# Performance work log

Measured on AMD Instinct MI355X. Metric: run time of the kernel, lower is better.

Reference implementation:

```python
import jax, jax.numpy as jnp
import numpy as np

EMBED = 1024
FF = 4096
LN_EPS = 1e-5

def _layernorm(x, gamma, beta):
    mu = jnp.mean(x, axis=-1, keepdims=True)
    var = jnp.var(x, axis=-1, keepdims=True)
    return (x - mu) * jax.lax.rsqrt(var + LN_EPS) * gamma + beta

def setup_inputs() -> dict:
    key = jax.random.key(0)
    ks = jax.random.split(key, 16)
    s = 1.0 / np.sqrt(EMBED)
    s2 = 1.0 / np.sqrt(FF)
    return {
        "x": jax.random.normal(ks[0], (8, 2048, EMBED), dtype=jnp.float32),
        "Wq": jax.random.uniform(ks[1], (EMBED, EMBED), jnp.float32, -s, s),
        "bq": jnp.zeros((EMBED,), jnp.float32),
        "Wk": jax.random.uniform(ks[2], (EMBED, EMBED), jnp.float32, -s, s),
        "bk": jnp.zeros((EMBED,), jnp.float32),
        "Wv": jax.random.uniform(ks[3], (EMBED, EMBED), jnp.float32, -s, s),
        "bv": jnp.zeros((EMBED,), jnp.float32),
        "Wo": jax.random.uniform(ks[4], (EMBED, EMBED), jnp.float32, -s, s),
        "bo": jnp.zeros((EMBED,), jnp.float32),
        "g1": jnp.ones((EMBED,), jnp.float32),
        "b1": jnp.zeros((EMBED,), jnp.float32),
        "g2": jnp.ones((EMBED,), jnp.float32),
        "b2": jnp.zeros((EMBED,), jnp.float32),
        "W1": jax.random.uniform(ks[5], (EMBED, FF), jnp.float32, -s, s),
        "bf1": jnp.zeros((FF,), jnp.float32),
        "W2": jax.random.uniform(ks[6], (FF, EMBED), jnp.float32, -s2, s2),
        "bf2": jnp.zeros((EMBED,), jnp.float32),
    }

def reference(x, Wq, bq, Wk, bk, Wv, bv, Wo, bo, g1, b1, g2, b2, W1, bf1, W2, bf2):
    # Single-head attention (heads arg unused in original forward)
    Q = jnp.einsum('bse,ef->bsf', x, Wq) + bq
    K = jnp.einsum('bse,ef->bsf', x, Wk) + bk
    V = jnp.einsum('bse,ef->bsf', x, Wv) + bv
    scale = 1.0 / jnp.sqrt(jnp.float32(EMBED))
    scores = jnp.einsum('bqe,bke->bqk', Q, K) * scale  # [B,S,S]
    attn = jax.nn.softmax(scores, axis=-1)
    attn_out = jnp.einsum('bqk,bke->bqe', attn, V)
    attn_out = jnp.einsum('bse,ef->bsf', attn_out, Wo) + bo
    # dropout is identity in eval mode
    h = _layernorm(x + attn_out, g1, b1)
    ffn = jnp.einsum('bsf,fh->bsh', jax.nn.relu(jnp.einsum('bse,eh->bsh', h, W1) + bf1), W2) + bf2
    return _layernorm(h + ffn, g2, b2)
```

## Files before the change

kernel.cpp:

```cpp
#include <hip/hip_runtime.h>


typedef __attribute__((ext_vector_type(4))) float  f32x4;
typedef __attribute__((ext_vector_type(8))) short  s16x8;
typedef __attribute__((ext_vector_type(4))) short  s16x4;
typedef unsigned short u16;
typedef unsigned int   u32;

__device__ __forceinline__ float bf2f(short s) {
  u32 u = ((u32)(u16)s) << 16;
  float f; __builtin_memcpy(&f, &u, 4); return f;
}
__device__ __forceinline__ short f2bf(float f) {
  u32 u; __builtin_memcpy(&u, &f, 4);
  u32 r = (u + 0x7fffu + ((u >> 16) & 1u)) >> 16;
  return (short)(u16)r;
}

__device__ __forceinline__ void gload16(const void* g, void* l) {
  __builtin_amdgcn_global_load_lds(
      (const __attribute__((address_space(1))) u32*)g,
      (__attribute__((address_space(3))) u32*)l, 16, 0, 0);
}

__device__ __forceinline__ void stage_half(const char* gop, long long ldb,
                                           long long rowbase, int tt, int h,
                                           u16* ldsop, int tid) {
#pragma unroll
  for (int l = 0; l < 2; ++l) {
    const int o   = (l * 512 + tid) * 16;
    const int rih = o >> 7;
    const int scb = (o & 127) ^ ((rih & 7) << 4);
    gload16(gop + (rowbase + h * 128 + rih) * ldb + (long long)tt * 128 + scb,
            (char*)ldsop + h * 16384 + o);
  }
}

#define SABUF(c) (SMEM + (c) * 16384)
#define SBBUF(c) (SMEM + 32768 + (c) * 16384)

#define RD_A(MH) do { _Pragma("unroll") for (int mi = 0; mi < 4; ++mi) { \
    const int row_ = wm * 64 + (MH) * 128 + mi * 16 + lr; \
    const int sw_ = (row_ & 7) << 4; const int rb_ = row_ << 7; \
    _Pragma("unroll") for (int kk = 0; kk < 2; ++kk) \
      af[mi][kk] = *(const s16x8*)(pa + rb_ + (((kk << 6) | (kg << 4)) ^ sw_)); } } while (0)

#define RD_B(NH) do { _Pragma("unroll") for (int nj = 0; nj < 2; ++nj) { \
    const int row_ = wn * 32 + (NH) * 128 + nj * 16 + lr; \
    const int sw_ = (row_ & 7) << 4; const int rb_ = row_ << 7; \
    _Pragma("unroll") for (int kk = 0; kk < 2; ++kk) \
      bf[NH][nj][kk] = *(const s16x8*)(pb + rb_ + (((kk << 6) | (kg << 4)) ^ sw_)); } } while (0)

#define MM(MH, NH) do { _Pragma("unroll") for (int kk = 0; kk < 2; ++kk) \
    _Pragma("unroll") for (int mi = 0; mi < 4; ++mi) \
    _Pragma("unroll") for (int nj = 0; nj < 2; ++nj) \
      acc[(MH) * 4 + mi][(NH) * 2 + nj] = __builtin_amdgcn_mfma_f32_16x16x32_bf16( \
        af[mi][kk], bf[NH][nj][kk], acc[(MH) * 4 + mi][(NH) * 2 + nj], 0, 0, 0); } while (0)

#define PH_SYNC do { __builtin_amdgcn_s_barrier(); \
    asm volatile("s_waitcnt lgkmcnt(0)"); \
    __builtin_amdgcn_sched_barrier(0); } while (0)

template<int MODE>
__global__ __launch_bounds__(512, 2)
void gemm256(const u16* __restrict__ A, const u16* __restrict__ BT,
             u16* __restrict__ C,
             const float* __restrict__ bias0, const float* __restrict__ bias1,
             const float* __restrict__ bias2, float* __restrict__ lsum,
             int M, int N, int K, float scale,
             long long sA, long long sB, long long sC) {
  __shared__ u16 SMEM[65536];

  const int gx = gridDim.x, gy = gridDim.y;
  const int nwg = gx * gy * gridDim.z;
  const int orig = (blockIdx.z * gy + blockIdx.y) * gx + blockIdx.x;
  const int q = nwg >> 3, r8 = nwg & 7;
  const int xcd = orig & 7, pos = orig >> 3;
  const int wg = (xcd < r8 ? xcd * (q + 1) : r8 * (q + 1) + (xcd - r8) * q) + pos;
  const int bz = wg / (gx * gy);
  const int rem = wg % (gx * gy);
  const long long bm = (long long)(rem / gx) * 256;
  const long long bn = (long long)(rem % gx) * 256;

  const char* Ag = (const char*)(A + (long long)bz * sA);
  const char* Bg = (const char*)(BT + (long long)bz * sB);
  u16* Cb = C + (long long)bz * sC;
  const long long ldb = (long long)K * 2;

  const int tid = threadIdx.x;
  const int lane = tid & 63, wid = tid >> 6;
  const int lr = lane & 15, kg = lane >> 4;
  const int wm = wid >> 2, wn = wid & 3;
  const int NT = K >> 6;

  f32x4 acc[8][4] = {};
  s16x8 af[4][2];
  s16x8 bf[2][2][2];

  stage_half(Ag, ldb, bm, 0, 0, SABUF(0), tid);
  stage_half(Bg, ldb, bn, 0, 0, SBBUF(0), tid);
  stage_half(Ag, ldb, bm, 0, 1, SABUF(0), tid);
  stage_half(Bg, ldb, bn, 0, 1, SBBUF(0), tid);
  stage_half(Ag, ldb, bm, 1, 0, SABUF(1), tid);
  stage_half(Bg, ldb, bn, 1, 0, SBBUF(1), tid);
  asm volatile("s_waitcnt vmcnt(4)");
  __builtin_amdgcn_s_barrier();

  for (int T = 0; T < NT; ++T) {
    const int c = T & 1, cn = c ^ 1;
    const char* pa = (const char*)SABUF(c);
    const char* pb = (const char*)SBBUF(c);

    RD_A(0); RD_B(0);
    if (T + 1 < NT) stage_half(Ag, ldb, bm, T + 1, 1, SABUF(cn), tid);
    PH_SYNC;
    __builtin_amdgcn_s_setprio(1); MM(0, 0); __builtin_amdgcn_s_setprio(0);
    __builtin_amdgcn_s_barrier();

    RD_B(1);
    if (T + 1 < NT) stage_half(Bg, ldb, bn, T + 1, 1, SBBUF(cn), tid);
    PH_SYNC;
    __builtin_amdgcn_s_setprio(1); MM(0, 1); __builtin_amdgcn_s_setprio(0);
    __builtin_amdgcn_s_barrier();

    RD_A(1);
    if (T + 2 < NT) stage_half(Ag, ldb, bm, T + 2, 0, SABUF(c), tid);
    PH_SYNC;
    __builtin_amdgcn_s_setprio(1); MM(1, 0); __builtin_amdgcn_s_setprio(0);
    __builtin_amdgcn_s_barrier();

    if (T + 2 < NT) stage_half(Bg, ldb, bn, T + 2, 0, SBBUF(c), tid);
    PH_SYNC;
    __builtin_amdgcn_s_setprio(1); MM(1, 1); __builtin_amdgcn_s_setprio(0);
    if (T + 2 < NT)      { asm volatile("s_waitcnt vmcnt(4)"); }
    else if (T + 1 < NT) { asm volatile("s_waitcnt vmcnt(0)"); }
    __builtin_amdgcn_s_barrier();
  }

  const long long zM = (long long)bz * M;
  u16* obase; long long ldc, bnl;
  const float* bptr = bias0;
  if (MODE == 5) {
    const int sel = (int)(bn >> 10);
    obase = C + (long long)sel * 16777216;
    ldc = 1024; bnl = bn & 1023;
    bptr = (sel == 0 ? bias0 : sel == 1 ? bias1 : bias2);
  } else { obase = Cb; ldc = N; bnl = bn; }

#pragma unroll
  for (int nh = 0; nh < 2; ++nh)
#pragma unroll
    for (int nj = 0; nj < 2; ++nj) {
      const int col = wn * 32 + nh * 128 + nj * 16 + lr;
      float bv = 0.f;
      if (MODE == 1 || MODE == 2 || MODE == 5) bv = bptr[bnl + col];
#pragma unroll
      for (int mh = 0; mh < 2; ++mh)
#pragma unroll
        for (int mi = 0; mi < 4; ++mi) {
          const int row0 = wm * 64 + mh * 128 + mi * 16 + kg * 4;
#pragma unroll
          for (int r = 0; r < 4; ++r) {
            float v = acc[mh * 4 + mi][nh * 2 + nj][r];
            if (MODE == 1 || MODE == 2 || MODE == 5) v = v * scale + bv;
            if (MODE == 2) v = fmaxf(v, 0.f);
            if (MODE == 3) v = __expf(v * scale);
            if (MODE == 4) v = v / lsum[zM + bm + row0 + r];
            SMEM[(row0 + r) * 256 + (col ^ (kg << 4))] = (u16)f2bf(v);
          }
        }
    }
  __syncthreads();
#pragma unroll
  for (int i = 0; i < 16; ++i) {
    const int o   = (i * 512 + tid) * 16;
    const int row = o >> 9;
    const int wb  = o & 511;
    const int gs  = (wb >> 4) ^ (((row >> 2) & 3) << 1);
    s16x8 d = *(const s16x8*)((const char*)SMEM + row * 512 + (gs << 4));
    if (MODE == 3) {
      float s = 0.f;
#pragma unroll
      for (int j = 0; j < 8; ++j) s += bf2f(d[j]);
#pragma unroll
      for (int off = 1; off < 32; off <<= 1) s += __shfl_xor(s, off);
      if ((lane & 31) == 0) atomicAdd(&lsum[zM + bm + row], s);
    }
    *(s16x8*)((char*)obase + (((long long)bm + row) * ldc + bnl) * 2 + wb) = d;
  }
}

__global__ __launch_bounds__(256) void prep(
    const float* __restrict__ x,  u16* __restrict__ XB,
    const float* __restrict__ Wq, const float* __restrict__ Wk,
    const float* __restrict__ Wv, const float* __restrict__ Wo,
    const float* __restrict__ W1, const float* __restrict__ W2,
    u16* __restrict__ WQT, u16* __restrict__ WKT, u16* __restrict__ WVT,
    u16* __restrict__ WOT, u16* __restrict__ W1T, u16* __restrict__ W2T) {
  __shared__ float tile[32][33];
  const int bid = blockIdx.x;
  const int t = threadIdx.x;
  if (bid < 16384) {
    const long long i = (long long)bid * 256 + t;
    f32x4 v = ((const f32x4*)x)[i];
    s16x4 o;
#pragma unroll
    for (int j = 0; j < 4; j++) o[j] = f2bf(v[j]);
    ((s16x4*)XB)[i] = o;
    return;
  }
  const float* in; u16* out; int R, C, tb;
  if (bid < 20480) {
    const int w = (bid - 16384) >> 10;
    tb = (bid - 16384) & 1023;
    in  = (w == 0 ? Wq : w == 1 ? Wk : w == 2 ? Wv : Wo);
    out = (w == 0 ? WQT : w == 1 ? WKT : w == 2 ? WVT : WOT);
    R = 1024; C = 1024;
  } else if (bid < 24576) {
    tb = bid - 20480; in = W1; out = W1T; R = 1024; C = 4096;
  } else {
    tb = bid - 24576; in = W2; out = W2T; R = 4096; C = 1024;
  }
  const int tpr = C >> 5;
  const int r0 = (tb / tpr) * 32, c0 = (tb % tpr) * 32;
  const int tx = t & 31, ty = t >> 5;
#pragma unroll
  for (int i = 0; i < 32; i += 8)
    tile[ty + i][tx] = in[(long long)(r0 + ty + i) * C + (c0 + tx)];
  __syncthreads();
#pragma unroll
  for (int i = 0; i < 32; i += 8)
    out[(long long)(c0 + ty + i) * R + (r0 + tx)] = (u16)f2bf(tile[tx][ty + i]);
}

__global__ __launch_bounds__(256) void transpose_bf16_bf16(const u16* __restrict__ in,
                                                           u16* __restrict__ out,
                                                           int R, int C,
                                                           long long isb, long long osb) {
  __shared__ u16 tile[32][33];
  in  += (long long)blockIdx.z * isb;
  out += (long long)blockIdx.z * osb;
  const int tx = threadIdx.x, ty = threadIdx.y;
  const int r0 = blockIdx.y * 32, c0 = blockIdx.x * 32;
#pragma unroll
  for (int i = 0; i < 32; i += 8)
    tile[ty + i][tx] = in[(long long)(r0 + ty + i) * C + (c0 + tx)];
  __syncthreads();
#pragma unroll
  for (int i = 0; i < 32; i += 8)
    out[(long long)(c0 + ty + i) * R + (r0 + tx)] = tile[tx][ty + i];
}

template<bool OUTF32>
__global__ __launch_bounds__(256) void ln_add(const u16* __restrict__ a,
                                              const u16* __restrict__ b,
                                              const float* __restrict__ g,
                                              const float* __restrict__ be,
                                              void* __restrict__ outp) {
  const long long row = blockIdx.x;
  const int t = threadIdx.x;
  s16x4 avv = ((const s16x4*)(a + row * 1024))[t];
  s16x4 bvv = ((const s16x4*)(b + row * 1024))[t];
  float v[4]; float sum = 0.f, ss = 0.f;
#pragma unroll
  for (int j = 0; j < 4; j++) { v[j] = bf2f(avv[j]) + bf2f(bvv[j]); sum += v[j]; ss += v[j] * v[j]; }
#pragma unroll
  for (int off = 32; off > 0; off >>= 1) { sum += __shfl_xor(sum, off); ss += __shfl_xor(ss, off); }
  __shared__ float red[8];
  if ((t & 63) == 0) { red[t >> 6] = sum; red[4 + (t >> 6)] = ss; }
  __syncthreads();
  sum = (red[0] + red[1]) + (red[2] + red[3]);
  ss  = (red[4] + red[5]) + (red[6] + red[7]);
  const float mu   = sum * (1.f / 1024.f);
  const float var  = ss * (1.f / 1024.f) - mu * mu;
  const float rstd = rsqrtf(var + 1e-5f);
  if (OUTF32) {
    f32x4 o;
#pragma unroll
    for (int j = 0; j < 4; j++) {
      const int c = t * 4 + j;
      o[j] = (v[j] - mu) * rstd * g[c] + be[c];
    }
    ((f32x4*)((float*)outp + row * 1024))[t] = o;
  } else {
    s16x4 o;
#pragma unroll
    for (int j = 0; j < 4; j++) {
      const int c = t * 4 + j;
      o[j] = f2bf((v[j] - mu) * rstd * g[c] + be[c]);
    }
    *(s16x4*)&((u16*)outp)[row * 1024 + t * 4] = o;
  }
}

extern "C" void kernel_launch(void* const* d_in, const int* in_sizes, int n_in,
                              void* d_out, int out_size, void* d_ws, size_t ws_size,
                              hipStream_t stream) {
  const float* x   = (const float*)d_in[0];
  const float* Wq  = (const float*)d_in[1];
  const float* bq  = (const float*)d_in[2];
  const float* Wk  = (const float*)d_in[3];
  const float* bk  = (const float*)d_in[4];
  const float* Wv  = (const float*)d_in[5];
  const float* bv  = (const float*)d_in[6];
  const float* Wo  = (const float*)d_in[7];
  const float* bo  = (const float*)d_in[8];
  const float* g1  = (const float*)d_in[9];
  const float* b1  = (const float*)d_in[10];
  const float* g2  = (const float*)d_in[11];
  const float* b2  = (const float*)d_in[12];
  const float* W1  = (const float*)d_in[13];
  const float* bf1 = (const float*)d_in[14];
  const float* W2  = (const float*)d_in[15];
  const float* bf2 = (const float*)d_in[16];
  float* out = (float*)d_out;

  char* ws = (char*)d_ws;
  u16* wsWQT = (u16*)(ws + 0);
  u16* wsWKT = (u16*)(ws + 2097152);
  u16* wsWVT = (u16*)(ws + 4194304);
  u16* wsWOT = (u16*)(ws + 6291456);
  u16* wsW1T = (u16*)(ws + 8388608);
  u16* wsW2T = (u16*)(ws + 16777216);
  u16* wsXB  = (u16*)(ws + 25165824);
  u16* wsQ   = (u16*)(ws + 58720256);
  u16* wsK   = (u16*)(ws + 92274688);
  u16* wsV   = (u16*)(ws + 125829120);
  u16* wsVT  = (u16*)(ws + 159383552);
  u16* wsS   = (u16*)(ws + 192937984);
  u16* wsAO  = wsQ;
  u16* wsAO2 = wsS;
  u16* wsH   = (u16*)(ws + 192937984 + 33554432);
  u16* wsHID = wsXB;
  u16* wsFFN = wsS;
  float* wsLSUM = (float*)wsV;

  const dim3 tb(32, 8, 1);
  const float inv_sqrt_e = 0.03125f;
  const float* nf = nullptr;
  float* nfm = nullptr;

  prep<<<28672, 256, 0, stream>>>(x, wsXB, Wq, Wk, Wv, Wo, W1, W2,
                                  wsWQT, wsWKT, wsWVT, wsWOT, wsW1T, wsW2T);

  gemm256<5><<<dim3(12, 64, 1), 512, 0, stream>>>(wsXB, wsWQT, wsQ, bq, bk, bv, nfm,
                                                  16384, 3072, 1024, 1.f, 0, 0, 0);

  transpose_bf16_bf16<<<dim3(32, 64, 8), tb, 0, stream>>>(wsV, wsVT, 2048, 1024, 2048LL * 1024, 1024LL * 2048);
  hipMemsetAsync(wsLSUM, 0, 16384 * sizeof(float), stream);

  gemm256<3><<<dim3(8, 8, 8), 512, 0, stream>>>(wsQ, wsK, wsS, nf, nf, nf, wsLSUM,
                                                2048, 2048, 1024, inv_sqrt_e,
                                                2048LL * 1024, 2048LL * 1024, 2048LL * 2048);

  gemm256<4><<<dim3(4, 8, 8), 512, 0, stream>>>(wsS, wsVT, wsAO, nf, nf, nf, wsLSUM,
                                                2048, 1024, 2048, 1.f,
                                                2048LL * 2048, 1024LL * 2048, 2048LL * 1024);
  gemm256<1><<<dim3(4, 64, 1), 512, 0, stream>>>(wsAO, wsWOT, wsAO2, bo, nf, nf, nfm,
                                                 16384, 1024, 1024, 1.f, 0, 0, 0);

  ln_add<false><<<16384, 256, 0, stream>>>(wsXB, wsAO2, g1, b1, wsH);

  gemm256<2><<<dim3(16, 64, 1), 512, 0, stream>>>(wsH, wsW1T, wsHID, bf1, nf, nf, nfm,
                                                  16384, 4096, 1024, 1.f, 0, 0, 0);

  gemm256<1><<<dim3(4, 64, 1), 512, 0, stream>>>(wsHID, wsW2T, wsFFN, bf2, nf, nf, nfm,
                                                 16384, 1024, 4096, 1.f, 0, 0, 0);

  ln_add<true><<<16384, 256, 0, stream>>>(wsH, wsFFN, g2, b2, out);

  (void)in_sizes; (void)n_in; (void)out_size; (void)ws_size;
}
```

Baseline: 614.3 us.

## Make GEMMs persistent with cross-tile prefetch and chunked epilogue

Converts the tiled GEMM into a persistent kernel launched with 256 workgroups that loop over output tiles in XCD-aware order. The next tile's first K-slices are prefetched into shared memory while the current tile finishes. The epilogue now writes 64-row chunks through the unused halves of the shared buffers, so output stores overlap with the next tile's loads. This targets per-tile prologue and epilogue bubbles and wave-quantization tails, at the cost of more barriers and register pressure.

After: 759.5 us. +23.6%, slower.

```diff
diff --git a/kernel.cpp b/kernel.cpp
--- a/kernel.cpp
+++ b/kernel.cpp
@@ -38,6 +38,8 @@
 
 #define SABUF(c) (SMEM + (c) * 16384)
 #define SBBUF(c) (SMEM + 32768 + (c) * 16384)
+#define EP0 (SMEM + 24576)
+#define EP1 (SMEM + 57344)
 
 #define RD_A(MH) do { _Pragma("unroll") for (int mi = 0; mi < 4; ++mi) { \
     const int row_ = wm * 64 + (MH) * 128 + mi * 16 + lr; \
@@ -61,132 +63,186 @@
     asm volatile("s_waitcnt lgkmcnt(0)"); \
     __builtin_amdgcn_sched_barrier(0); } while (0)
 
+__device__ __forceinline__ int perm8(int orig, int ntiles) {
+  const int q = ntiles >> 3, r8 = ntiles & 7;
+  const int xcd = orig & 7, pos = orig >> 3;
+  return (xcd < r8 ? xcd * (q + 1) : r8 * (q + 1) + (xcd - r8) * q) + pos;
+}
+
 template<int MODE>
 __global__ __launch_bounds__(512, 2)
-void gemm256(const u16* __restrict__ A, const u16* __restrict__ BT,
-             u16* __restrict__ C,
-             const float* __restrict__ bias0, const float* __restrict__ bias1,
-             const float* __restrict__ bias2, float* __restrict__ lsum,
-             int M, int N, int K, float scale,
-             long long sA, long long sB, long long sC) {
+void gemm256p(const u16* __restrict__ A, const u16* __restrict__ BT,
+              u16* __restrict__ C,
+              const float* __restrict__ bias0, const float* __restrict__ bias1,
+              const float* __restrict__ bias2, float* __restrict__ lsum,
+              int M, int N, int K, int NBZ,
+              long long sA, long long sB, long long sC, float scale) {
   __shared__ u16 SMEM[65536];
 
-  const int gx = gridDim.x, gy = gridDim.y;
-  const int nwg = gx * gy * gridDim.z;
-  const int orig = (blockIdx.z * gy + blockIdx.y) * gx + blockIdx.x;
-  const int q = nwg >> 3, r8 = nwg & 7;
-  const int xcd = orig & 7, pos = orig >> 3;
-  const int wg = (xcd < r8 ? xcd * (q + 1) : r8 * (q + 1) + (xcd - r8) * q) + pos;
-  const int bz = wg / (gx * gy);
-  const int rem = wg % (gx * gy);
-  const long long bm = (long long)(rem / gx) * 256;
-  const long long bn = (long long)(rem % gx) * 256;
-
-  const char* Ag = (const char*)(A + (long long)bz * sA);
-  const char* Bg = (const char*)(BT + (long long)bz * sB);
-  u16* Cb = C + (long long)bz * sC;
+  const int tn = N >> 8;
+  const int tilesPerZ = (M >> 8) * tn;
+  const int ntiles = NBZ * tilesPerZ;
+  const int NT = K >> 6;
   const long long ldb = (long long)K * 2;
+  const int G = gridDim.x;
 
   const int tid = threadIdx.x;
   const int lane = tid & 63, wid = tid >> 6;
   const int lr = lane & 15, kg = lane >> 4;
   const int wm = wid >> 2, wn = wid & 3;
-  const int NT = K >> 6;
+
+  const char *curA, *curB, *nxtA, *nxtB;
+  long long curBm, curBn, nxtBm, nxtBn;
+  int curZ, nxtZ;
+  auto mk = [&](int tl, const char*& ag, const char*& bg,
+                long long& bm, long long& bn, int& z) {
+    z = tl / tilesPerZ;
+    const int rm = tl - z * tilesPerZ;
+    bm = (long long)(rm / tn) << 8;
+    bn = (long long)(rm - (rm / tn) * tn) << 8;
+    ag = (const char*)(A + (long long)z * sA);
+    bg = (const char*)(BT + (long long)z * sB);
+  };
+
+  int jt = blockIdx.x;
+  mk(perm8(jt, ntiles), curA, curB, curBm, curBn, curZ);
+  bool hasNext = (jt + G) < ntiles;
+  if (hasNext) mk(perm8(jt + G, ntiles), nxtA, nxtB, nxtBm, nxtBn, nxtZ);
+  else { nxtA = curA; nxtB = curB; nxtBm = curBm; nxtBn = curBn; nxtZ = curZ; }
 
   f32x4 acc[8][4] = {};
   s16x8 af[4][2];
   s16x8 bf[2][2][2];
 
-  stage_half(Ag, ldb, bm, 0, 0, SABUF(0), tid);
-  stage_half(Bg, ldb, bn, 0, 0, SBBUF(0), tid);
-  stage_half(Ag, ldb, bm, 0, 1, SABUF(0), tid);
-  stage_half(Bg, ldb, bn, 0, 1, SBBUF(0), tid);
-  stage_half(Ag, ldb, bm, 1, 0, SABUF(1), tid);
-  stage_half(Bg, ldb, bn, 1, 0, SBBUF(1), tid);
+  stage_half(curA, ldb, curBm, 0, 0, SABUF(0), tid);
+  stage_half(curB, ldb, curBn, 0, 0, SBBUF(0), tid);
+  stage_half(curA, ldb, curBm, 0, 1, SABUF(0), tid);
+  stage_half(curB, ldb, curBn, 0, 1, SBBUF(0), tid);
+  stage_half(curA, ldb, curBm, 1, 0, SABUF(1), tid);
+  stage_half(curB, ldb, curBn, 1, 0, SBBUF(1), tid);
   asm volatile("s_waitcnt vmcnt(4)");
   __builtin_amdgcn_s_barrier();
 
-  for (int T = 0; T < NT; ++T) {
-    const int c = T & 1, cn = c ^ 1;
-    const char* pa = (const char*)SABUF(c);
-    const char* pb = (const char*)SBBUF(c);
-
-    RD_A(0); RD_B(0);
-    if (T + 1 < NT) stage_half(Ag, ldb, bm, T + 1, 1, SABUF(cn), tid);
-    PH_SYNC;
-    __builtin_amdgcn_s_setprio(1); MM(0, 0); __builtin_amdgcn_s_setprio(0);
-    __builtin_amdgcn_s_barrier();
-
-    RD_B(1);
-    if (T + 1 < NT) stage_half(Bg, ldb, bn, T + 1, 1, SBBUF(cn), tid);
-    PH_SYNC;
-    __builtin_amdgcn_s_setprio(1); MM(0, 1); __builtin_amdgcn_s_setprio(0);
-    __builtin_amdgcn_s_barrier();
-
-    RD_A(1);
-    if (T + 2 < NT) stage_half(Ag, ldb, bm, T + 2, 0, SABUF(c), tid);
-    PH_SYNC;
-    __builtin_amdgcn_s_setprio(1); MM(1, 0); __builtin_amdgcn_s_setprio(0);
-    __builtin_amdgcn_s_barrier();
-
-    if (T + 2 < NT) stage_half(Bg, ldb, bn, T + 2, 0, SBBUF(c), tid);
-    PH_SYNC;
-    __builtin_amdgcn_s_setprio(1); MM(1, 1); __builtin_amdgcn_s_setprio(0);
-    if (T + 2 < NT)      { asm volatile("s_waitcnt vmcnt(4)"); }
-    else if (T + 1 < NT) { asm volatile("s_waitcnt vmcnt(0)"); }
-    __builtin_amdgcn_s_barrier();
-  }
-
-  const long long zM = (long long)bz * M;
-  u16* obase; long long ldc, bnl;
-  const float* bptr = bias0;
-  if (MODE == 5) {
-    const int sel = (int)(bn >> 10);
-    obase = C + (long long)sel * 16777216;
-    ldc = 1024; bnl = bn & 1023;
-    bptr = (sel == 0 ? bias0 : sel == 1 ? bias1 : bias2);
-  } else { obase = Cb; ldc = N; bnl = bn; }
-
-#pragma unroll
-  for (int nh = 0; nh < 2; ++nh)
-#pragma unroll
-    for (int nj = 0; nj < 2; ++nj) {
-      const int col = wn * 32 + nh * 128 + nj * 16 + lr;
-      float bv = 0.f;
-      if (MODE == 1 || MODE == 2 || MODE == 5) bv = bptr[bnl + col];
-#pragma unroll
-      for (int mh = 0; mh < 2; ++mh)
-#pragma unroll
-        for (int mi = 0; mi < 4; ++mi) {
-          const int row0 = wm * 64 + mh * 128 + mi * 16 + kg * 4;
-#pragma unroll
-          for (int r = 0; r < 4; ++r) {
-            float v = acc[mh * 4 + mi][nh * 2 + nj][r];
-            if (MODE == 1 || MODE == 2 || MODE == 5) v = v * scale + bv;
-            if (MODE == 2) v = fmaxf(v, 0.f);
-            if (MODE == 3) v = __expf(v * scale);
-            if (MODE == 4) v = v / lsum[zM + bm + row0 + r];
-            SMEM[(row0 + r) * 256 + (col ^ (kg << 4))] = (u16)f2bf(v);
+  for (;;) {
+    for (int T = 0; T < NT; ++T) {
+      const int c = T & 1, cn = c ^ 1;
+      const char* pa = (const char*)SABUF(c);
+      const char* pb = (const char*)SBBUF(c);
+
+      const bool in1 = (T + 1 < NT), in2 = (T + 2 < NT);
+      const bool v1 = in1 || hasNext, v2 = in2 || hasNext;
+      const char* a1 = in1 ? curA : nxtA;  const char* b1 = in1 ? curB : nxtB;
+      const long long m1 = in1 ? curBm : nxtBm, n1 = in1 ? curBn : nxtBn;
+      const int tk1 = in1 ? T + 1 : 0;
+      const char* a2 = in2 ? curA : nxtA;  const char* b2 = in2 ? curB : nxtB;
+      const long long m2 = in2 ? curBm : nxtBm, n2 = in2 ? curBn : nxtBn;
+      const int tk2 = in2 ? T + 2 : T + 2 - NT;
+
+      RD_A(0); RD_B(0);
+      if (v1) stage_half(a1, ldb, m1, tk1, 1, SABUF(cn), tid);
+      PH_SYNC;
+      __builtin_amdgcn_s_setprio(1); MM(0, 0); __builtin_amdgcn_s_setprio(0);
+      __builtin_amdgcn_s_barrier();
+
+      RD_B(1);
+      if (v1) stage_half(b1, ldb, n1, tk1, 1, SBBUF(cn), tid);
+      PH_SYNC;
+      __builtin_amdgcn_s_setprio(1); MM(0, 1); __builtin_amdgcn_s_setprio(0);
+      __builtin_amdgcn_s_barrier();
+
+      RD_A(1);
+      if (v2) stage_half(a2, ldb, m2, tk2, 0, SABUF(c), tid);
+      PH_SYNC;
+      __builtin_amdgcn_s_setprio(1); MM(1, 0); __builtin_amdgcn_s_setprio(0);
+      __builtin_amdgcn_s_barrier();
+
+      if (v2) stage_half(b2, ldb, n2, tk2, 0, SBBUF(c), tid);
+      PH_SYNC;
+      __builtin_amdgcn_s_setprio(1); MM(1, 1); __builtin_amdgcn_s_setprio(0);
+      if (v2)      { asm volatile("s_waitcnt vmcnt(4)"); }
+      else if (v1) { asm volatile("s_waitcnt vmcnt(0)"); }
+      __builtin_amdgcn_s_barrier();
+    }
+
+    {
+      u16* Cb = C + (long long)curZ * sC;
+      const long long zM = (long long)curZ * M;
+      u16* obase; long long ldc, bnl;
+      const float* bptr = bias0;
+      if (MODE == 5) {
+        const int sel = (int)(curBn >> 10);
+        obase = C + (long long)sel * 16777216;
+        ldc = 1024; bnl = curBn & 1023;
+        bptr = (sel == 0 ? bias0 : sel == 1 ? bias1 : bias2);
+      } else { obase = Cb; ldc = N; bnl = curBn; }
+
+      float bvv[2][2];
+      if (MODE == 1 || MODE == 2 || MODE == 5) {
+#pragma unroll
+        for (int nh = 0; nh < 2; ++nh)
+#pragma unroll
+          for (int nj = 0; nj < 2; ++nj)
+            bvv[nh][nj] = bptr[bnl + wn * 32 + nh * 128 + nj * 16 + lr];
+      }
+
+#pragma unroll
+      for (int b = 0; b < 4; ++b) {
+        const int mh = b >> 1;
+        if (wm == (b & 1)) {
+#pragma unroll
+          for (int nh = 0; nh < 2; ++nh)
+#pragma unroll
+            for (int nj = 0; nj < 2; ++nj) {
+              const int col = wn * 32 + nh * 128 + nj * 16 + lr;
+#pragma unroll
+              for (int mi = 0; mi < 4; ++mi)
+#pragma unroll
+                for (int r = 0; r < 4; ++r) {
+                  const int lrow = mi * 16 + kg * 4 + r;
+                  float v = acc[mh * 4 + mi][nh * 2 + nj][r];
+                  if (MODE == 1 || MODE == 2 || MODE == 5) v = v * scale + bvv[nh][nj];
+                  if (MODE == 2) v = fmaxf(v, 0.f);
+                  if (MODE == 3) v = __expf(v * scale);
+                  if (MODE == 4) v = v / lsum[zM + curBm + b * 64 + lrow];
+                  u16* ep = (lrow < 32) ? EP0 : EP1;
+                  ep[(lrow & 31) * 256 + (col ^ (kg << 4))] = (u16)f2bf(v);
+                }
+            }
+        }
+        asm volatile("s_waitcnt lgkmcnt(0)" ::: "memory");
+        __builtin_amdgcn_sched_barrier(0);
+        __builtin_amdgcn_s_barrier();
+#pragma unroll
+        for (int i = 0; i < 4; ++i) {
+          const int o    = (i * 512 + tid) * 16;
+          const int lrow = o >> 9;
+          const int wb   = o & 511;
+          const int gs   = (wb >> 4) ^ (((lrow >> 2) & 3) << 1);
+          const u16* ep  = (lrow < 32) ? EP0 : EP1;
+          s16x8 d = *(const s16x8*)((const char*)ep + (lrow & 31) * 512 + (gs << 4));
+          if (MODE == 3) {
+            float s = 0.f;
+#pragma unroll
+            for (int j = 0; j < 8; ++j) s += bf2f(d[j]);
+#pragma unroll
+            for (int off = 1; off < 32; off <<= 1) s += __shfl_xor(s, off);
+            if ((lane & 31) == 0) atomicAdd(&lsum[zM + curBm + b * 64 + lrow], s);
           }
+          *(s16x8*)((char*)obase + (((long long)curBm + b * 64 + lrow) * ldc + bnl) * 2 + wb) = d;
         }
+        __builtin_amdgcn_s_barrier();
+      }
     }
-  __syncthreads();
-#pragma unroll
-  for (int i = 0; i < 16; ++i) {
-    const int o   = (i * 512 + tid) * 16;
-    const int row = o >> 9;
-    const int wb  = o & 511;
-    const int gs  = (wb >> 4) ^ (((row >> 2) & 3) << 1);
-    s16x8 d = *(const s16x8*)((const char*)SMEM + row * 512 + (gs << 4));
-    if (MODE == 3) {
-      float s = 0.f;
-#pragma unroll
-      for (int j = 0; j < 8; ++j) s += bf2f(d[j]);
-#pragma unroll
-      for (int off = 1; off < 32; off <<= 1) s += __shfl_xor(s, off);
-      if ((lane & 31) == 0) atomicAdd(&lsum[zM + bm + row], s);
-    }
-    *(s16x8*)((char*)obase + (((long long)bm + row) * ldc + bnl) * 2 + wb) = d;
+
+    jt += G;
+    if (jt >= ntiles) break;
+    curA = nxtA; curB = nxtB; curBm = nxtBm; curBn = nxtBn; curZ = nxtZ;
+    hasNext = (jt + G) < ntiles;
+    if (hasNext) mk(perm8(jt + G, ntiles), nxtA, nxtB, nxtBm, nxtBn, nxtZ);
+#pragma unroll
+    for (int i = 0; i < 8; ++i)
+#pragma unroll
+      for (int j = 0; j < 4; ++j) acc[i][j] = (f32x4){0.f, 0.f, 0.f, 0.f};
   }
 }
 
@@ -343,29 +399,30 @@
   prep<<<28672, 256, 0, stream>>>(x, wsXB, Wq, Wk, Wv, Wo, W1, W2,
                                   wsWQT, wsWKT, wsWVT, wsWOT, wsW1T, wsW2T);
 
-  gemm256<5><<<dim3(12, 64, 1), 512, 0, stream>>>(wsXB, wsWQT, wsQ, bq, bk, bv, nfm,
-                                                  16384, 3072, 1024, 1.f, 0, 0, 0);
+  gemm256p<5><<<256, 512, 0, stream>>>(wsXB, wsWQT, wsQ, bq, bk, bv, nfm,
+                                       16384, 3072, 1024, 1, 0, 0, 0, 1.f);
 
   transpose_bf16_bf16<<<dim3(32, 64, 8), tb, 0, stream>>>(wsV, wsVT, 2048, 1024, 2048LL * 1024, 1024LL * 2048);
   hipMemsetAsync(wsLSUM, 0, 16384 * sizeof(float), stream);
 
-  gemm256<3><<<dim3(8, 8, 8), 512, 0, stream>>>(wsQ, wsK, wsS, nf, nf, nf, wsLSUM,
-                                                2048, 2048, 1024, inv_sqrt_e,
-                                                2048LL * 1024, 2048LL * 1024, 2048LL * 2048);
-
-  gemm256<4><<<dim3(4, 8, 8), 512, 0, stream>>>(wsS, wsVT, wsAO, nf, nf, nf, wsLSUM,
-                                                2048, 1024, 2048, 1.f,
-                                                2048LL * 2048, 1024LL * 2048, 2048LL * 1024);
-  gemm256<1><<<dim3(4, 64, 1), 512, 0, stream>>>(wsAO, wsWOT, wsAO2, bo, nf, nf, nfm,
-                                                 16384, 1024, 1024, 1.f, 0, 0, 0);
+  gemm256p<3><<<256, 512, 0, stream>>>(wsQ, wsK, wsS, nf, nf, nf, wsLSUM,
+                                       2048, 2048, 1024, 8,
+                                       2048LL * 1024, 2048LL * 1024, 2048LL * 2048, inv_sqrt_e);
+
+  gemm256p<4><<<256, 512, 0, stream>>>(wsS, wsVT, wsAO, nf, nf, nf, wsLSUM,
+                                       2048, 1024, 2048, 8,
+                                       2048LL * 2048, 1024LL * 2048, 2048LL * 1024, 1.f);
+
+  gemm256p<1><<<256, 512, 0, stream>>>(wsAO, wsWOT, wsAO2, bo, nf, nf, nfm,
+                                       16384, 1024, 1024, 1, 0, 0, 0, 1.f);
 
   ln_add<false><<<16384, 256, 0, stream>>>(wsXB, wsAO2, g1, b1, wsH);
 
-  gemm256<2><<<dim3(16, 64, 1), 512, 0, stream>>>(wsH, wsW1T, wsHID, bf1, nf, nf, nfm,
-                                                  16384, 4096, 1024, 1.f, 0, 0, 0);
-
-  gemm256<1><<<dim3(4, 64, 1), 512, 0, stream>>>(wsHID, wsW2T, wsFFN, bf2, nf, nf, nfm,
-                                                 16384, 1024, 4096, 1.f, 0, 0, 0);
+  gemm256p<2><<<256, 512, 0, stream>>>(wsH, wsW1T, wsHID, bf1, nf, nf, nfm,
+                                       16384, 4096, 1024, 1, 0, 0, 0, 1.f);
+
+  gemm256p<1><<<256, 512, 0, stream>>>(wsHID, wsW2T, wsFFN, bf2, nf, nf, nfm,
+                                       16384, 1024, 4096, 1, 0, 0, 0, 1.f);
 
   ln_add<true><<<16384, 256, 0, stream>>>(wsH, wsFFN, g2, b2, out);
 
```

## Compute V transposed directly via swapped-operand GEMM, drop transpose kernel

Applied to the files above, without the earlier changes.

The fused QKV projection now computes only Q and K. V^T is produced directly by a new batched GEMM mode that multiplies Wv^T by the activations and adds a per-row bias. This removes the separate bf16 transpose kernel and the write and re-read of V. It relies on MODE 5's output layout placing K at the old wsK offset. It also adds a second, smaller GEMM launch with different tiling.

Result: no change. 603.8 us (-1.7%).

```diff
diff --git a/kernel.cpp b/kernel.cpp
--- a/kernel.cpp
+++ b/kernel.cpp
@@ -166,6 +166,7 @@
             if (MODE == 2) v = fmaxf(v, 0.f);
             if (MODE == 3) v = __expf(v * scale);
             if (MODE == 4) v = v / lsum[zM + bm + row0 + r];
+            if (MODE == 6) v = v * scale + bias0[bm + row0 + r];
             SMEM[(row0 + r) * 256 + (col ^ (kg << 4))] = (u16)f2bf(v);
           }
         }
@@ -231,24 +232,6 @@
 #pragma unroll
   for (int i = 0; i < 32; i += 8)
     out[(long long)(c0 + ty + i) * R + (r0 + tx)] = (u16)f2bf(tile[tx][ty + i]);
-}
-
-__global__ __launch_bounds__(256) void transpose_bf16_bf16(const u16* __restrict__ in,
-                                                           u16* __restrict__ out,
-                                                           int R, int C,
-                                                           long long isb, long long osb) {
-  __shared__ u16 tile[32][33];
-  in  += (long long)blockIdx.z * isb;
-  out += (long long)blockIdx.z * osb;
-  const int tx = threadIdx.x, ty = threadIdx.y;
-  const int r0 = blockIdx.y * 32, c0 = blockIdx.x * 32;
-#pragma unroll
-  for (int i = 0; i < 32; i += 8)
-    tile[ty + i][tx] = in[(long long)(r0 + ty + i) * C + (c0 + tx)];
-  __syncthreads();
-#pragma unroll
-  for (int i = 0; i < 32; i += 8)
-    out[(long long)(c0 + ty + i) * R + (r0 + tx)] = tile[tx][ty + i];
 }
 
 template<bool OUTF32>
@@ -324,8 +307,6 @@
   u16* wsW2T = (u16*)(ws + 16777216);
   u16* wsXB  = (u16*)(ws + 25165824);
   u16* wsQ   = (u16*)(ws + 58720256);
-  u16* wsK   = (u16*)(ws + 92274688);
-  u16* wsV   = (u16*)(ws + 125829120);
   u16* wsVT  = (u16*)(ws + 159383552);
   u16* wsS   = (u16*)(ws + 192937984);
   u16* wsAO  = wsQ;
@@ -333,23 +314,24 @@
   u16* wsH   = (u16*)(ws + 192937984 + 33554432);
   u16* wsHID = wsXB;
   u16* wsFFN = wsS;
-  float* wsLSUM = (float*)wsV;
-
-  const dim3 tb(32, 8, 1);
+  float* wsLSUM = (float*)(ws + 125829120);
+
   const float inv_sqrt_e = 0.03125f;
   const float* nf = nullptr;
   float* nfm = nullptr;
 
   prep<<<28672, 256, 0, stream>>>(x, wsXB, Wq, Wk, Wv, Wo, W1, W2,
                                   wsWQT, wsWKT, wsWVT, wsWOT, wsW1T, wsW2T);
-
-  gemm256<5><<<dim3(12, 64, 1), 512, 0, stream>>>(wsXB, wsWQT, wsQ, bq, bk, bv, nfm,
-                                                  16384, 3072, 1024, 1.f, 0, 0, 0);
-
-  transpose_bf16_bf16<<<dim3(32, 64, 8), tb, 0, stream>>>(wsV, wsVT, 2048, 1024, 2048LL * 1024, 1024LL * 2048);
   hipMemsetAsync(wsLSUM, 0, 16384 * sizeof(float), stream);
 
-  gemm256<3><<<dim3(8, 8, 8), 512, 0, stream>>>(wsQ, wsK, wsS, nf, nf, nf, wsLSUM,
+  gemm256<5><<<dim3(8, 64, 1), 512, 0, stream>>>(wsXB, wsWQT, wsQ, bq, bk, nf, nfm,
+                                                 16384, 2048, 1024, 1.f, 0, 0, 0);
+
+  gemm256<6><<<dim3(8, 4, 8), 512, 0, stream>>>(wsWVT, wsXB, wsVT, bv, nf, nf, nfm,
+                                                1024, 2048, 1024, 1.f,
+                                                0, 2048LL * 1024, 1024LL * 2048);
+
+  gemm256<3><<<dim3(8, 8, 8), 512, 0, stream>>>(wsQ, (u16*)(ws + 92274688), wsS, nf, nf, nf, wsLSUM,
                                                 2048, 2048, 1024, inv_sqrt_e,
                                                 2048LL * 1024, 2048LL * 1024, 2048LL * 2048);
 
```
